# Optimization experiments

Hardware: AMD Instinct MI355X
Metric: run time of the kernel (lower is better)

The kernel has to match this reference:

```python
import jax, jax.numpy as jnp
import numpy as np

EMBED_DIM = 1024
NUM_HEADS = 16
ROTARY_THETA = 10000.0


def _rotate_half(t):
    d = t.shape[-1] // 2
    t1, t2 = t[..., :d], t[..., d:]
    return jnp.concatenate([-t2, t1], axis=-1)


def _rope_cos_sin(seq_len, head_dim, dtype):
    # inv_freq over even indices, standard RoPE
    inv_freq = 1.0 / (ROTARY_THETA ** (jnp.arange(0, head_dim, 2, dtype=jnp.float32) / head_dim))
    freqs = jnp.arange(seq_len, dtype=jnp.float32)[:, None] * inv_freq[None, :]  # (S, D/2)
    emb = jnp.concatenate([freqs, freqs], axis=-1)  # (S, D)
    # broadcast over (b, s, h, d)
    return jnp.cos(emb).astype(dtype)[None, :, None, :], jnp.sin(emb).astype(dtype)[None, :, None, :]


def setup_inputs() -> dict:
    key = jax.random.key(0)
    ks = jax.random.split(key, 4)
    B, S, E = 2, 2048, EMBED_DIM
    scale = 1.0 / np.sqrt(E)
    return {
        "x": jax.random.normal(ks[0], (B, S, E), dtype=jnp.float32),
        "attention_mask": jnp.zeros((B, 1, 1, S), dtype=jnp.float32),
        "Wq": jax.random.normal(ks[1], (E, E), dtype=jnp.float32) * scale,
        "bq": jnp.zeros((E,), dtype=jnp.float32),
        "Wk": jax.random.normal(ks[2], (E, E), dtype=jnp.float32) * scale,
        "bk": jnp.zeros((E,), dtype=jnp.float32),
        "Wv": jax.random.normal(ks[3], (E, E), dtype=jnp.float32) * scale,
        "bv": jnp.zeros((E,), dtype=jnp.float32),
    }


def reference(x, attention_mask, Wq, bq, Wk, bk, Wv, bv):
    B, S, E = x.shape
    H = NUM_HEADS
    D = E // H

    q = (x @ Wq + bq).reshape(B, S, H, D)
    k = (x @ Wk + bk).reshape(B, S, H, D)
    v = (x @ Wv + bv).reshape(B, S, H, D)

    cos, sin = _rope_cos_sin(S, D, q.dtype)
    q = q * cos + _rotate_half(q) * sin
    k = k * cos + _rotate_half(k) * sin

    # attention_mask: additive padding bias (b,1,1,k) broadcast over heads & queries
    scores = jnp.einsum("bqhd,bkhd->bhqk", q, k) / jnp.sqrt(jnp.asarray(D, dtype=q.dtype))
    scores = scores + attention_mask  # broadcasts to (b,h,q,k)
    attn = jax.nn.softmax(scores, axis=-1)
    out = jnp.einsum("bhqk,bkhd->bqhd", attn, v)
    return out.reshape(B, S, E)
```

## Files before the change

### kernel.cpp

```cpp
#include <hip/hip_runtime.h>

typedef __attribute__((ext_vector_type(8)))  short bf16x8;
typedef __attribute__((ext_vector_type(4)))  float f32x4;
typedef __attribute__((ext_vector_type(16))) float f32x16;
typedef __attribute__((ext_vector_type(4)))  unsigned u32x4;
typedef __attribute__((ext_vector_type(4)))  _Float16 f16x4;

#define B_  2
#define S_  2048
#define H_  16
#define D_  64
#define E_  1024
#define M_  (B_*S_)
#define L2E 1.44269504f

__device__ __forceinline__ unsigned short f2bf(float f){
  unsigned x = __builtin_bit_cast(unsigned, f);
  x += 0x7fffu + ((x >> 16) & 1u);
  return (unsigned short)(x >> 16);
}
__device__ __forceinline__ unsigned pk_bf16(float lo, float hi){
  unsigned short a = __builtin_bit_cast(unsigned short, (__bf16)lo);
  unsigned short b = __builtin_bit_cast(unsigned short, (__bf16)hi);
  return (unsigned)a | ((unsigned)b << 16);
}

#define GLD16(gp, lp) __builtin_amdgcn_global_load_lds( \
    (const __attribute__((address_space(1))) unsigned*)(gp), \
    (__attribute__((address_space(3))) unsigned*)(lp), 16, 0, 0)

__global__ __launch_bounds__(256) void k_tables(const float* __restrict__ mask,
                                                float* ct, float* st, float* maskC){
  int i = blockIdx.x*256 + threadIdx.x;
  int s = i >> 5, f = i & 31;
  float invf = powf(10000.0f, -(float)f / 32.0f);
  float ph = (float)s * invf;
  ct[i] = cosf(ph);
  st[i] = sinf(ph);
  if(i < B_*S_) maskC[i] = fmaf(mask[i], L2E, -17.0f);
}

__global__ __launch_bounds__(256) void k_cvt(const float* __restrict__ in, short* __restrict__ out){
  int i = (blockIdx.x*256 + threadIdx.x)*4;
  float4 v = *(const float4*)(in + i);
  typedef __attribute__((ext_vector_type(4))) short s16x4;
  s16x4 o = { (short)f2bf(v.x), (short)f2bf(v.y), (short)f2bf(v.z), (short)f2bf(v.w) };
  *(s16x4*)(out + i) = o;
}

__global__ __launch_bounds__(256) void k_wt(const float* __restrict__ Wq, const float* __restrict__ Wk,
                                            const float* __restrict__ Wv, short* __restrict__ wt){
  const float* W = blockIdx.z==0 ? Wq : (blockIdx.z==1 ? Wk : Wv);
  short* out = wt + (size_t)blockIdx.z*E_*E_;
  __shared__ short tile[64][72];
  int nb = blockIdx.x*64, kb = blockIdx.y*64;
  int t = threadIdx.x;
  {
    int r = t>>2, c0 = (t&3)*16;
    const float* src = W + (size_t)(kb+r)*E_ + nb + c0;
    #pragma unroll
    for(int i=0;i<4;i++){
      float4 v = *(const float4*)(src + i*4);
      tile[r][c0+i*4+0] = (short)f2bf(v.x);
      tile[r][c0+i*4+1] = (short)f2bf(v.y);
      tile[r][c0+i*4+2] = (short)f2bf(v.z);
      tile[r][c0+i*4+3] = (short)f2bf(v.w);
    }
  }
  __syncthreads();
  {
    int n = t>>2, k0 = (t&3)*16;
    short* dst = out + (size_t)(nb+n)*E_ + kb + k0;
    bf16x8 o0, o1;
    #pragma unroll
    for(int i=0;i<8;i++){ o0[i] = tile[k0+i][n]; o1[i] = tile[k0+8+i][n]; }
    *(bf16x8*)dst = o0;
    *(bf16x8*)(dst+8) = o1;
  }
}

__global__ __launch_bounds__(256) void k_gemm(const short* __restrict__ A, const short* __restrict__ WT,
                                              const float* __restrict__ biasq, const float* __restrict__ biask,
                                              const float* __restrict__ biasv,
                                              short* __restrict__ oq, short* __restrict__ ok, short* __restrict__ ov,
                                              const float* __restrict__ cost, const float* __restrict__ sint){
  const int z = blockIdx.z;
  const short* Bw = WT + (size_t)z*E_*E_;
  const float* bias = z==0 ? biasq : (z==1 ? biask : biasv);
  short* out = z==0 ? oq : (z==1 ? ok : ov);
  __shared__ short As[128*32];
  __shared__ short Bs[128*32];
  const int t = threadIdx.x, lane = t & 63, wid = t >> 6;
  const int mb = blockIdx.x*128, nb = blockIdx.y*128;
  const int wm = (wid>>1)*64, wn = (wid&1)*64;
  f32x4 acc[4][4] = {};
  for(int kt=0; kt<E_/32; kt++){
    __syncthreads();
    {
      int f0 = t, f1 = t + 256;
      GLD16(A  + (size_t)(mb + (f0>>2))*E_ + kt*32 + (f0&3)*8, &As[f0*8]);
      GLD16(A  + (size_t)(mb + (f1>>2))*E_ + kt*32 + (f1&3)*8, &As[f1*8]);
      GLD16(Bw + (size_t)(nb + (f0>>2))*E_ + kt*32 + (f0&3)*8, &Bs[f0*8]);
      GLD16(Bw + (size_t)(nb + (f1>>2))*E_ + kt*32 + (f1&3)*8, &Bs[f1*8]);
    }
    __syncthreads();
    bf16x8 af[4], bfv[4];
    #pragma unroll
    for(int mf=0; mf<4; mf++)
      af[mf] = *(const bf16x8*)&As[(wm + mf*16 + (lane&15))*32 + (lane>>4)*8];
    #pragma unroll
    for(int nf=0; nf<4; nf++)
      bfv[nf] = *(const bf16x8*)&Bs[(wn + nf*16 + (lane&15))*32 + (lane>>4)*8];
    #pragma unroll
    for(int mf=0; mf<4; mf++)
      #pragma unroll
      for(int nf=0; nf<4; nf++)
        acc[mf][nf] = __builtin_amdgcn_mfma_f32_16x16x32_bf16(af[mf], bfv[nf], acc[mf][nf], 0, 0, 0);
  }
  const int col16 = lane & 15, rg = lane >> 4;
  float bvs[4];
  #pragma unroll
  for(int nf=0; nf<4; nf++) bvs[nf] = bias[nb + wn + nf*16 + col16];
  if(z == 2){
    #pragma unroll
    for(int mf=0; mf<4; mf++)
      #pragma unroll
      for(int nf=0; nf<4; nf++)
        #pragma unroll
        for(int r=0; r<4; r++){
          int row = mb + wm + mf*16 + rg*4 + r;
          out[(size_t)row*E_ + nb + wn + nf*16 + col16] = (short)f2bf(acc[mf][nf][r] + bvs[nf]);
        }
  } else {
    const float qs = (z==0) ? (0.125f*L2E) : 1.0f;
    #pragma unroll
    for(int mf=0; mf<4; mf++)
      #pragma unroll
      for(int r=0; r<4; r++){
        int row = mb + wm + mf*16 + rg*4 + r;
        int srow = row & (S_-1);
        const float* cb = cost + (size_t)srow*32;
        const float* sb = sint + (size_t)srow*32;
        #pragma unroll
        for(int nf=0; nf<2; nf++){
          int d = nf*16 + col16;
          float c = cb[d], sn = sb[d];
          float x0 = acc[mf][nf][r]   + bvs[nf];
          float x1 = acc[mf][nf+2][r] + bvs[nf+2];
          out[(size_t)row*E_ + nb + wn + nf*16 + col16]     = (short)f2bf((x0*c - x1*sn)*qs);
          out[(size_t)row*E_ + nb + wn + (nf+2)*16 + col16] = (short)f2bf((x1*c + x0*sn)*qs);
        }
      }
  }
}

__global__ __launch_bounds__(256) void k_vt(const short* __restrict__ v, short* __restrict__ vt){
  __shared__ short tl[64][72];
  const int b = blockIdx.z, h = blockIdx.y, s0 = blockIdx.x*64;
  const int t = threadIdx.x;
  {
    int r = t>>2, c0 = (t&3)*16;
    const short* src = v + ((size_t)(b*S_ + s0 + r)*H_ + h)*D_ + c0;
    *(bf16x8*)&tl[r][c0]   = *(const bf16x8*)src;
    *(bf16x8*)&tl[r][c0+8] = *(const bf16x8*)(src+8);
  }
  __syncthreads();
  {
    int d = t>>2, t0 = (t&3)*16;
    short* dst = vt + ((size_t)(b*H_ + h)*D_ + d)*S_ + s0 + t0;
    bf16x8 o0, o1;
    #pragma unroll
    for(int i=0;i<8;i++){ o0[i] = tl[t0+i][d]; o1[i] = tl[t0+8+i][d]; }
    *(bf16x8*)dst = o0;
    *(bf16x8*)(dst+8) = o1;
  }
}

__global__ __launch_bounds__(256,4) void k_attn(
    const short* __restrict__ qg, const short* __restrict__ kg,
    const short* __restrict__ vtg, const float* __restrict__ maskC,
    float* __restrict__ o0g, _Float16* __restrict__ o1g, float* __restrict__ lpart){
  __shared__ short Ks[2][64*72];
  __shared__ short Vs[2][64*72];
  const int b = blockIdx.z, h = blockIdx.y;
  const int qb = blockIdx.x >> 1, sp = blockIdx.x & 1;
  const int tid = threadIdx.x, wid = tid>>6, lane = tid&63;
  const int l31 = lane & 31, hl = lane >> 5;
  const int qw = qb*128 + wid*32;
  const int rr = tid>>3, ch = tid&7;
  const int kb0 = sp*16;
  const int NT = 16;

  bf16x8 qf[4];
  {
    const short* qp = qg + ((size_t)(b*S_ + qw + l31)*H_ + h)*D_;
    #pragma unroll
    for(int dk=0; dk<4; dk++)
      qf[dk] = *(const bf16x8*)(qp + dk*16 + hl*8);
  }
  f32x16 O0 = {}, O1 = {};
  float l_run = 0.f;
  const float* mrow = maskC + (size_t)b*S_;

  bf16x8 ka, kc, va, vc;
#define LOADT(kb) { \
    const short* ks_ = kg + ((size_t)(b*S_ + (kb)*64 + rr)*H_ + h)*D_ + ch*8; \
    ka = *(const bf16x8*)ks_;  kc = *(const bf16x8*)(ks_ + 32*H_*D_); \
    const short* vs_ = vtg + ((size_t)(b*H_ + h)*D_ + rr)*S_ + (kb)*64 + ch*8; \
    va = *(const bf16x8*)vs_;  vc = *(const bf16x8*)(vs_ + 32*S_); }
#define WRITET(pp) { \
    *(bf16x8*)&Ks[pp][rr*72 + ch*8]      = ka; \
    *(bf16x8*)&Ks[pp][(rr+32)*72 + ch*8] = kc; \
    *(bf16x8*)&Vs[pp][rr*72 + ch*8]      = va; \
    *(bf16x8*)&Vs[pp][(rr+32)*72 + ch*8] = vc; }

  LOADT(kb0);
  WRITET(0);
  LOADT(kb0+1);
  __syncthreads();

  int p = 0;
  for(int tt=0; tt<NT; tt++){
    f32x16 s0 = {}, s1 = {};
    #pragma unroll
    for(int dk=0; dk<4; dk++){
      bf16x8 kf0 = *(const bf16x8*)&Ks[p][(l31)*72 + dk*16 + hl*8];
      bf16x8 kf1 = *(const bf16x8*)&Ks[p][(32+l31)*72 + dk*16 + hl*8];
      s0 = __builtin_amdgcn_mfma_f32_32x32x16_bf16(kf0, qf[dk], s0, 0,0,0);
      s1 = __builtin_amdgcn_mfma_f32_32x32x16_bf16(kf1, qf[dk], s1, 0,0,0);
    }
    {
      const float* mt = mrow + (kb0+tt)*64 + hl*4;
      #pragma unroll
      for(int bb=0; bb<4; bb++){
        f32x4 mv0 = *(const f32x4*)(mt + bb*8);
        f32x4 mv1 = *(const f32x4*)(mt + 32 + bb*8);
        #pragma unroll
        for(int a=0; a<4; a++){ s0[bb*4+a] += mv0[a]; s1[bb*4+a] += mv1[a]; }
      }
    }
    #pragma unroll
    for(int i=0;i<16;i++) s0[i] = __builtin_amdgcn_exp2f(s0[i]);
    #pragma unroll
    for(int i=0;i<16;i++) s1[i] = __builtin_amdgcn_exp2f(s1[i]);
    float la=0.f, lb=0.f, lc=0.f, ld=0.f;
    #pragma unroll
    for(int i=0;i<4;i++){
      la += s0[i];   lb += s0[4+i];  lc += s0[8+i];  ld += s0[12+i];
      la += s1[i];   lb += s1[4+i];  lc += s1[8+i];  ld += s1[12+i];
    }
    float ls = (la+lb)+(lc+ld);
    ls += __shfl_xor(ls, 32);
    l_run += ls;

    unsigned w0a[8], w1a[8];
    #pragma unroll
    for(int c=0;c<8;c++){
      int base = (c&3)*4;
      float p0 = (c & 4) ? s1[base+0] : s0[base+0];
      float p1 = (c & 4) ? s1[base+1] : s0[base+1];
      float p2 = (c & 4) ? s1[base+2] : s0[base+2];
      float p3 = (c & 4) ? s1[base+3] : s0[base+3];
      w0a[c] = pk_bf16(p0, p1);
      w1a[c] = pk_bf16(p2, p3);
    }

    if(tt+1 < NT){
      WRITET(p^1);
      if(tt+2 < NT) LOADT(kb0+tt+2);
    }

    #pragma unroll
    for(int ksl=0; ksl<4; ksl++){
      unsigned a0 = w0a[2*ksl], b0 = w0a[2*ksl+1];
      unsigned a1 = w1a[2*ksl], b1 = w1a[2*ksl+1];
      asm("v_permlane32_swap_b32 %0, %1" : "+v"(a0), "+v"(b0));
      asm("v_permlane32_swap_b32 %0, %1" : "+v"(a1), "+v"(b1));
      u32x4 pw = { a0, a1, b0, b1 };
      bf16x8 pf = __builtin_bit_cast(bf16x8, pw);
      bf16x8 vf0 = *(const bf16x8*)&Vs[p][(l31)*72 + ksl*16 + hl*8];
      bf16x8 vf1 = *(const bf16x8*)&Vs[p][(32+l31)*72 + ksl*16 + hl*8];
      O0 = __builtin_amdgcn_mfma_f32_32x32x16_bf16(pf, vf0, O0, 0,0,0);
      O1 = __builtin_amdgcn_mfma_f32_32x32x16_bf16(pf, vf1, O1, 0,0,0);
    }
    __syncthreads();
    p ^= 1;
  }
#undef LOADT
#undef WRITET

  if(sp == 0){
    #pragma unroll
    for(int bb=0; bb<4; bb++)
      #pragma unroll
      for(int a=0; a<4; a++){
        int qrow = qw + a + 8*bb + 4*hl;
        float* op = o0g + ((size_t)(b*S_ + qrow)*H_ + h)*D_;
        op[l31]      = O0[bb*4+a];
        op[32 + l31] = O1[bb*4+a];
      }
  } else {
    #pragma unroll
    for(int bb=0; bb<4; bb++)
      #pragma unroll
      for(int a=0; a<4; a++){
        int qrow = qw + a + 8*bb + 4*hl;
        _Float16* op = o1g + ((size_t)(b*S_ + qrow)*H_ + h)*D_;
        op[l31]      = (_Float16)O0[bb*4+a];
        op[32 + l31] = (_Float16)O1[bb*4+a];
      }
  }
  if(lane < 32)
    lpart[(size_t)sp*(M_*H_) + (size_t)(b*S_ + qw + l31)*H_ + h] = l_run;
}

__global__ __launch_bounds__(256) void k_comb(float* __restrict__ out, const _Float16* __restrict__ o1,
                                              const float* __restrict__ lpart){
  int i = blockIdx.x*256 + threadIdx.x;
  int idx = i*4;
  int lidx = idx >> 6;
  float linv = 1.f / (lpart[lidx] + lpart[M_*H_ + lidx]);
  f32x4 a = *(f32x4*)(out + idx);
  f16x4 bb = *(const f16x4*)(o1 + idx);
  f32x4 r = { (a[0] + (float)bb[0])*linv, (a[1] + (float)bb[1])*linv,
              (a[2] + (float)bb[2])*linv, (a[3] + (float)bb[3])*linv };
  *(f32x4*)(out + idx) = r;
}

extern "C" void kernel_launch(void* const* d_in, const int* in_sizes, int n_in,
                              void* d_out, int out_size, void* d_ws, size_t ws_size,
                              hipStream_t stream){
  (void)in_sizes; (void)n_in; (void)out_size; (void)ws_size;
  const float* x    = (const float*)d_in[0];
  const float* mask = (const float*)d_in[1];
  const float* Wq   = (const float*)d_in[2];
  const float* bq   = (const float*)d_in[3];
  const float* Wk   = (const float*)d_in[4];
  const float* bk   = (const float*)d_in[5];
  const float* Wv   = (const float*)d_in[6];
  const float* bv   = (const float*)d_in[7];
  float* out = (float*)d_out;
  char* ws = (char*)d_ws;
  float* cost  = (float*)(ws);
  float* sint  = (float*)(ws + (256u<<10));
  float* maskC = (float*)(ws + (512u<<10));
  float* lpart = (float*)(ws + (768u<<10));
  short* xb    = (short*)(ws + (2u<<20));
  short* wt    = (short*)(ws + (10u<<20));
  short* qb    = (short*)(ws + (16u<<20));
  short* kb    = (short*)(ws + (24u<<20));
  short* vb    = (short*)(ws + (32u<<20));
  short* vtb   = xb;
  _Float16* o1 = (_Float16*)vb;

  k_tables<<<dim3(256), dim3(256), 0, stream>>>(mask, cost, sint, maskC);
  k_cvt<<<dim3(4096), dim3(256), 0, stream>>>(x, xb);
  k_wt<<<dim3(16,16,3), dim3(256), 0, stream>>>(Wq, Wk, Wv, wt);
  k_gemm<<<dim3(32,8,3), dim3(256), 0, stream>>>(xb, wt, bq, bk, bv, qb, kb, vb, cost, sint);
  k_vt<<<dim3(32,16,2), dim3(256), 0, stream>>>(vb, vtb);
  k_attn<<<dim3(32,16,2), dim3(256), 0, stream>>>(qb, kb, vtb, maskC, out, o1, lpart);
  k_comb<<<dim3(4096), dim3(256), 0, stream>>>(out, o1, lpart);
}
```

Before: 128.0 us.

## Fuse split-KV attention combine in-block, write V transposed from GEMM, merge prologue kernels

The attention kernel now runs three 256-thread groups per block, each covering about a third of the KV tiles. Partial outputs and row sums are reduced through shared memory, which removes the separate combine kernel and the fp16 partial buffer. The V projection epilogue writes directly in transposed layout, removing the k_vt kernel, and the table setup is folded into the x conversion. The mask transform moves into the attention inner loop. In exchange, the per-group loop is single-buffered with two barriers per tile and the block has 768 threads with a larger shared footprint, which may hurt latency hiding and occupancy.

After: 287.8 us. 2.25x slower.

```diff
diff --git a/kernel.cpp b/kernel.cpp
--- a/kernel.cpp
+++ b/kernel.cpp
@@ -1,10 +1,10 @@
 #include <hip/hip_runtime.h>
 
 typedef __attribute__((ext_vector_type(8)))  short bf16x8;
+typedef __attribute__((ext_vector_type(4)))  short s16x4;
 typedef __attribute__((ext_vector_type(4)))  float f32x4;
 typedef __attribute__((ext_vector_type(16))) float f32x16;
 typedef __attribute__((ext_vector_type(4)))  unsigned u32x4;
-typedef __attribute__((ext_vector_type(4)))  _Float16 f16x4;
 
 #define B_  2
 #define S_  2048
@@ -29,23 +29,20 @@
     (const __attribute__((address_space(1))) unsigned*)(gp), \
     (__attribute__((address_space(3))) unsigned*)(lp), 16, 0, 0)
 
-__global__ __launch_bounds__(256) void k_tables(const float* __restrict__ mask,
-                                                float* ct, float* st, float* maskC){
+__global__ __launch_bounds__(256) void k_cvt(const float* __restrict__ in, short* __restrict__ out,
+                                             float* ct, float* st){
   int i = blockIdx.x*256 + threadIdx.x;
-  int s = i >> 5, f = i & 31;
-  float invf = powf(10000.0f, -(float)f / 32.0f);
-  float ph = (float)s * invf;
-  ct[i] = cosf(ph);
-  st[i] = sinf(ph);
-  if(i < B_*S_) maskC[i] = fmaf(mask[i], L2E, -17.0f);
-}
-
-__global__ __launch_bounds__(256) void k_cvt(const float* __restrict__ in, short* __restrict__ out){
-  int i = (blockIdx.x*256 + threadIdx.x)*4;
-  float4 v = *(const float4*)(in + i);
-  typedef __attribute__((ext_vector_type(4))) short s16x4;
+  if(i < S_*32){
+    int s = i >> 5, f = i & 31;
+    float invf = powf(10000.0f, -(float)f / 32.0f);
+    float ph = (float)s * invf;
+    ct[i] = cosf(ph);
+    st[i] = sinf(ph);
+  }
+  int j = i*4;
+  float4 v = *(const float4*)(in + j);
   s16x4 o = { (short)f2bf(v.x), (short)f2bf(v.y), (short)f2bf(v.z), (short)f2bf(v.w) };
-  *(s16x4*)(out + i) = o;
+  *(s16x4*)(out + j) = o;
 }
 
 __global__ __launch_bounds__(256) void k_wt(const float* __restrict__ Wq, const float* __restrict__ Wk,
@@ -82,12 +79,11 @@
 __global__ __launch_bounds__(256) void k_gemm(const short* __restrict__ A, const short* __restrict__ WT,
                                               const float* __restrict__ biasq, const float* __restrict__ biask,
                                               const float* __restrict__ biasv,
-                                              short* __restrict__ oq, short* __restrict__ ok, short* __restrict__ ov,
+                                              short* __restrict__ oq, short* __restrict__ ok, short* __restrict__ ovt,
                                               const float* __restrict__ cost, const float* __restrict__ sint){
   const int z = blockIdx.z;
   const short* Bw = WT + (size_t)z*E_*E_;
   const float* bias = z==0 ? biasq : (z==1 ? biask : biasv);
-  short* out = z==0 ? oq : (z==1 ? ok : ov);
   __shared__ short As[128*32];
   __shared__ short Bs[128*32];
   const int t = threadIdx.x, lane = t & 63, wid = t >> 6;
@@ -123,15 +119,20 @@
   for(int nf=0; nf<4; nf++) bvs[nf] = bias[nb + wn + nf*16 + col16];
   if(z == 2){
     #pragma unroll
-    for(int mf=0; mf<4; mf++)
-      #pragma unroll
-      for(int nf=0; nf<4; nf++)
-        #pragma unroll
-        for(int r=0; r<4; r++){
-          int row = mb + wm + mf*16 + rg*4 + r;
-          out[(size_t)row*E_ + nb + wn + nf*16 + col16] = (short)f2bf(acc[mf][nf][r] + bvs[nf]);
-        }
+    for(int mf=0; mf<4; mf++){
+      int row0 = mb + wm + mf*16 + rg*4;
+      int bb2 = row0 >> 11, ss = row0 & (S_-1);
+      #pragma unroll
+      for(int nf=0; nf<4; nf++){
+        int e = nb + wn + nf*16 + col16;
+        int hh = e >> 6, dd = e & 63;
+        s16x4 w = { (short)f2bf(acc[mf][nf][0]+bvs[nf]), (short)f2bf(acc[mf][nf][1]+bvs[nf]),
+                    (short)f2bf(acc[mf][nf][2]+bvs[nf]), (short)f2bf(acc[mf][nf][3]+bvs[nf]) };
+        *(s16x4*)(ovt + ((size_t)(bb2*H_+hh)*D_+dd)*S_ + ss) = w;
+      }
+    }
   } else {
+    short* out = (z==0) ? oq : ok;
     const float qs = (z==0) ? (0.125f*L2E) : 1.0f;
     #pragma unroll
     for(int mf=0; mf<4; mf++)
@@ -154,42 +155,21 @@
   }
 }
 
-__global__ __launch_bounds__(256) void k_vt(const short* __restrict__ v, short* __restrict__ vt){
-  __shared__ short tl[64][72];
-  const int b = blockIdx.z, h = blockIdx.y, s0 = blockIdx.x*64;
-  const int t = threadIdx.x;
-  {
-    int r = t>>2, c0 = (t&3)*16;
-    const short* src = v + ((size_t)(b*S_ + s0 + r)*H_ + h)*D_ + c0;
-    *(bf16x8*)&tl[r][c0]   = *(const bf16x8*)src;
-    *(bf16x8*)&tl[r][c0+8] = *(const bf16x8*)(src+8);
-  }
-  __syncthreads();
-  {
-    int d = t>>2, t0 = (t&3)*16;
-    short* dst = vt + ((size_t)(b*H_ + h)*D_ + d)*S_ + s0 + t0;
-    bf16x8 o0, o1;
-    #pragma unroll
-    for(int i=0;i<8;i++){ o0[i] = tl[t0+i][d]; o1[i] = tl[t0+8+i][d]; }
-    *(bf16x8*)dst = o0;
-    *(bf16x8*)(dst+8) = o1;
-  }
-}
-
-__global__ __launch_bounds__(256,4) void k_attn(
+__global__ __launch_bounds__(768, 6) void k_attn(
     const short* __restrict__ qg, const short* __restrict__ kg,
-    const short* __restrict__ vtg, const float* __restrict__ maskC,
-    float* __restrict__ o0g, _Float16* __restrict__ o1g, float* __restrict__ lpart){
-  __shared__ short Ks[2][64*72];
-  __shared__ short Vs[2][64*72];
+    const short* __restrict__ vtg, const float* __restrict__ mask,
+    float* __restrict__ outg){
+  __shared__ short smem[3*2*64*72];
   const int b = blockIdx.z, h = blockIdx.y;
-  const int qb = blockIdx.x >> 1, sp = blockIdx.x & 1;
   const int tid = threadIdx.x, wid = tid>>6, lane = tid&63;
+  const int g = wid>>2, w = wid&3;
   const int l31 = lane & 31, hl = lane >> 5;
-  const int qw = qb*128 + wid*32;
-  const int rr = tid>>3, ch = tid&7;
-  const int kb0 = sp*16;
-  const int NT = 16;
+  const int qw = blockIdx.x*128 + w*32;
+  const int tg = tid & 255, rr = tg>>3, ch = tg&7;
+  const int kb0 = g*11;
+  const int NT  = (g==2) ? 10 : 11;
+  short* Ksg = smem + g*9216;
+  short* Vsg = Ksg + 4608;
 
   bf16x8 qf[4];
   {
@@ -200,7 +180,7 @@
   }
   f32x16 O0 = {}, O1 = {};
   float l_run = 0.f;
-  const float* mrow = maskC + (size_t)b*S_;
+  const float* mrow = mask + (size_t)b*S_;
 
   bf16x8 ka, kc, va, vc;
 #define LOADT(kb) { \
@@ -208,123 +188,123 @@
     ka = *(const bf16x8*)ks_;  kc = *(const bf16x8*)(ks_ + 32*H_*D_); \
     const short* vs_ = vtg + ((size_t)(b*H_ + h)*D_ + rr)*S_ + (kb)*64 + ch*8; \
     va = *(const bf16x8*)vs_;  vc = *(const bf16x8*)(vs_ + 32*S_); }
-#define WRITET(pp) { \
-    *(bf16x8*)&Ks[pp][rr*72 + ch*8]      = ka; \
-    *(bf16x8*)&Ks[pp][(rr+32)*72 + ch*8] = kc; \
-    *(bf16x8*)&Vs[pp][rr*72 + ch*8]      = va; \
-    *(bf16x8*)&Vs[pp][(rr+32)*72 + ch*8] = vc; }
+#define WRITET() { \
+    *(bf16x8*)&Ksg[rr*72 + ch*8]      = ka; \
+    *(bf16x8*)&Ksg[(rr+32)*72 + ch*8] = kc; \
+    *(bf16x8*)&Vsg[rr*72 + ch*8]      = va; \
+    *(bf16x8*)&Vsg[(rr+32)*72 + ch*8] = vc; }
 
   LOADT(kb0);
-  WRITET(0);
-  LOADT(kb0+1);
+  WRITET();
   __syncthreads();
 
-  int p = 0;
-  for(int tt=0; tt<NT; tt++){
-    f32x16 s0 = {}, s1 = {};
-    #pragma unroll
-    for(int dk=0; dk<4; dk++){
-      bf16x8 kf0 = *(const bf16x8*)&Ks[p][(l31)*72 + dk*16 + hl*8];
-      bf16x8 kf1 = *(const bf16x8*)&Ks[p][(32+l31)*72 + dk*16 + hl*8];
-      s0 = __builtin_amdgcn_mfma_f32_32x32x16_bf16(kf0, qf[dk], s0, 0,0,0);
-      s1 = __builtin_amdgcn_mfma_f32_32x32x16_bf16(kf1, qf[dk], s1, 0,0,0);
-    }
-    {
-      const float* mt = mrow + (kb0+tt)*64 + hl*4;
-      #pragma unroll
-      for(int bb=0; bb<4; bb++){
-        f32x4 mv0 = *(const f32x4*)(mt + bb*8);
-        f32x4 mv1 = *(const f32x4*)(mt + 32 + bb*8);
+  for(int tt=0; tt<11; tt++){
+    if(tt+1 < NT) LOADT(kb0+tt+1);
+    if(tt < NT){
+      f32x16 s0 = {}, s1 = {};
+      #pragma unroll
+      for(int dk=0; dk<4; dk++){
+        bf16x8 kf0 = *(const bf16x8*)&Ksg[(l31)*72 + dk*16 + hl*8];
+        bf16x8 kf1 = *(const bf16x8*)&Ksg[(32+l31)*72 + dk*16 + hl*8];
+        s0 = __builtin_amdgcn_mfma_f32_32x32x16_bf16(kf0, qf[dk], s0, 0,0,0);
+        s1 = __builtin_amdgcn_mfma_f32_32x32x16_bf16(kf1, qf[dk], s1, 0,0,0);
+      }
+      {
+        const float* mt = mrow + (kb0+tt)*64 + hl*4;
         #pragma unroll
-        for(int a=0; a<4; a++){ s0[bb*4+a] += mv0[a]; s1[bb*4+a] += mv1[a]; }
-      }
-    }
-    #pragma unroll
-    for(int i=0;i<16;i++) s0[i] = __builtin_amdgcn_exp2f(s0[i]);
-    #pragma unroll
-    for(int i=0;i<16;i++) s1[i] = __builtin_amdgcn_exp2f(s1[i]);
-    float la=0.f, lb=0.f, lc=0.f, ld=0.f;
-    #pragma unroll
-    for(int i=0;i<4;i++){
-      la += s0[i];   lb += s0[4+i];  lc += s0[8+i];  ld += s0[12+i];
-      la += s1[i];   lb += s1[4+i];  lc += s1[8+i];  ld += s1[12+i];
-    }
-    float ls = (la+lb)+(lc+ld);
-    ls += __shfl_xor(ls, 32);
-    l_run += ls;
-
-    unsigned w0a[8], w1a[8];
-    #pragma unroll
-    for(int c=0;c<8;c++){
-      int base = (c&3)*4;
-      float p0 = (c & 4) ? s1[base+0] : s0[base+0];
-      float p1 = (c & 4) ? s1[base+1] : s0[base+1];
-      float p2 = (c & 4) ? s1[base+2] : s0[base+2];
-      float p3 = (c & 4) ? s1[base+3] : s0[base+3];
-      w0a[c] = pk_bf16(p0, p1);
-      w1a[c] = pk_bf16(p2, p3);
-    }
-
-    if(tt+1 < NT){
-      WRITET(p^1);
-      if(tt+2 < NT) LOADT(kb0+tt+2);
-    }
-
-    #pragma unroll
-    for(int ksl=0; ksl<4; ksl++){
-      unsigned a0 = w0a[2*ksl], b0 = w0a[2*ksl+1];
-      unsigned a1 = w1a[2*ksl], b1 = w1a[2*ksl+1];
-      asm("v_permlane32_swap_b32 %0, %1" : "+v"(a0), "+v"(b0));
-      asm("v_permlane32_swap_b32 %0, %1" : "+v"(a1), "+v"(b1));
-      u32x4 pw = { a0, a1, b0, b1 };
-      bf16x8 pf = __builtin_bit_cast(bf16x8, pw);
-      bf16x8 vf0 = *(const bf16x8*)&Vs[p][(l31)*72 + ksl*16 + hl*8];
-      bf16x8 vf1 = *(const bf16x8*)&Vs[p][(32+l31)*72 + ksl*16 + hl*8];
-      O0 = __builtin_amdgcn_mfma_f32_32x32x16_bf16(pf, vf0, O0, 0,0,0);
-      O1 = __builtin_amdgcn_mfma_f32_32x32x16_bf16(pf, vf1, O1, 0,0,0);
-    }
-    __syncthreads();
-    p ^= 1;
+        for(int bb=0; bb<4; bb++){
+          f32x4 mv0 = *(const f32x4*)(mt + bb*8);
+          f32x4 mv1 = *(const f32x4*)(mt + 32 + bb*8);
+          #pragma unroll
+          for(int a=0; a<4; a++){
+            s0[bb*4+a] += fmaf(mv0[a], L2E, -17.0f);
+            s1[bb*4+a] += fmaf(mv1[a], L2E, -17.0f);
+          }
+        }
+      }
+      #pragma unroll
+      for(int i=0;i<16;i++) s0[i] = __builtin_amdgcn_exp2f(s0[i]);
+      #pragma unroll
+      for(int i=0;i<16;i++) s1[i] = __builtin_amdgcn_exp2f(s1[i]);
+      float la=0.f, lb=0.f, lc=0.f, ld=0.f;
+      #pragma unroll
+      for(int i=0;i<4;i++){
+        la += s0[i];   lb += s0[4+i];  lc += s0[8+i];  ld += s0[12+i];
+        la += s1[i];   lb += s1[4+i];  lc += s1[8+i];  ld += s1[12+i];
+      }
+      float ls = (la+lb)+(lc+ld);
+      ls += __shfl_xor(ls, 32);
+      l_run += ls;
+
+      unsigned w0a[8], w1a[8];
+      #pragma unroll
+      for(int c=0;c<8;c++){
+        int base = (c&3)*4;
+        float p0 = (c & 4) ? s1[base+0] : s0[base+0];
+        float p1 = (c & 4) ? s1[base+1] : s0[base+1];
+        float p2 = (c & 4) ? s1[base+2] : s0[base+2];
+        float p3 = (c & 4) ? s1[base+3] : s0[base+3];
+        w0a[c] = pk_bf16(p0, p1);
+        w1a[c] = pk_bf16(p2, p3);
+      }
+      #pragma unroll
+      for(int ksl=0; ksl<4; ksl++){
+        unsigned a0 = w0a[2*ksl], b0 = w0a[2*ksl+1];
+        unsigned a1 = w1a[2*ksl], b1 = w1a[2*ksl+1];
+        asm("v_permlane32_swap_b32 %0, %1" : "+v"(a0), "+v"(b0));
+        asm("v_permlane32_swap_b32 %0, %1" : "+v"(a1), "+v"(b1));
+        u32x4 pw = { a0, a1, b0, b1 };
+        bf16x8 pf = __builtin_bit_cast(bf16x8, pw);
+        bf16x8 vf0 = *(const bf16x8*)&Vsg[(l31)*72 + ksl*16 + hl*8];
+        bf16x8 vf1 = *(const bf16x8*)&Vsg[(32+l31)*72 + ksl*16 + hl*8];
+        O0 = __builtin_amdgcn_mfma_f32_32x32x16_bf16(pf, vf0, O0, 0,0,0);
+        O1 = __builtin_amdgcn_mfma_f32_32x32x16_bf16(pf, vf1, O1, 0,0,0);
+      }
+    }
+    __syncthreads();
+    if(tt+1 < NT) WRITET();
+    __syncthreads();
   }
 #undef LOADT
 #undef WRITET
 
-  if(sp == 0){
+  float* ex  = (float*)smem;
+  float* exl = (float*)smem + 4*32*64;
+  #pragma unroll
+  for(int src=1; src<=2; src++){
+    if(g == src){
+      #pragma unroll
+      for(int r=0;r<16;r++){
+        ex[(w*32 + r)*64 + lane]      = O0[r];
+        ex[(w*32 + 16 + r)*64 + lane] = O1[r];
+      }
+      if(lane < 32) exl[w*32 + lane] = l_run;
+    }
+    __syncthreads();
+    if(g == 0){
+      #pragma unroll
+      for(int r=0;r<16;r++){
+        O0[r] += ex[(w*32 + r)*64 + lane];
+        O1[r] += ex[(w*32 + 16 + r)*64 + lane];
+      }
+      if(lane < 32) l_run += exl[w*32 + lane];
+    }
+    __syncthreads();
+  }
+
+  if(g == 0){
+    float linv = 1.f / l_run;
     #pragma unroll
     for(int bb=0; bb<4; bb++)
       #pragma unroll
       for(int a=0; a<4; a++){
+        float li = __shfl(linv, a + 8*bb + 4*hl);
         int qrow = qw + a + 8*bb + 4*hl;
-        float* op = o0g + ((size_t)(b*S_ + qrow)*H_ + h)*D_;
-        op[l31]      = O0[bb*4+a];
-        op[32 + l31] = O1[bb*4+a];
-      }
-  } else {
-    #pragma unroll
-    for(int bb=0; bb<4; bb++)
-      #pragma unroll
-      for(int a=0; a<4; a++){
-        int qrow = qw + a + 8*bb + 4*hl;
-        _Float16* op = o1g + ((size_t)(b*S_ + qrow)*H_ + h)*D_;
-        op[l31]      = (_Float16)O0[bb*4+a];
-        op[32 + l31] = (_Float16)O1[bb*4+a];
-      }
-  }
-  if(lane < 32)
-    lpart[(size_t)sp*(M_*H_) + (size_t)(b*S_ + qw + l31)*H_ + h] = l_run;
-}
-
-__global__ __launch_bounds__(256) void k_comb(float* __restrict__ out, const _Float16* __restrict__ o1,
-                                              const float* __restrict__ lpart){
-  int i = blockIdx.x*256 + threadIdx.x;
-  int idx = i*4;
-  int lidx = idx >> 6;
-  float linv = 1.f / (lpart[lidx] + lpart[M_*H_ + lidx]);
-  f32x4 a = *(f32x4*)(out + idx);
-  f16x4 bb = *(const f16x4*)(o1 + idx);
-  f32x4 r = { (a[0] + (float)bb[0])*linv, (a[1] + (float)bb[1])*linv,
-              (a[2] + (float)bb[2])*linv, (a[3] + (float)bb[3])*linv };
-  *(f32x4*)(out + idx) = r;
+        float* op = outg + ((size_t)(b*S_ + qrow)*H_ + h)*D_;
+        op[l31]      = O0[bb*4+a] * li;
+        op[32 + l31] = O1[bb*4+a] * li;
+      }
+  }
 }
 
 extern "C" void kernel_launch(void* const* d_in, const int* in_sizes, int n_in,
@@ -341,23 +321,16 @@
   const float* bv   = (const float*)d_in[7];
   float* out = (float*)d_out;
   char* ws = (char*)d_ws;
-  float* cost  = (float*)(ws);
-  float* sint  = (float*)(ws + (256u<<10));
-  float* maskC = (float*)(ws + (512u<<10));
-  float* lpart = (float*)(ws + (768u<<10));
-  short* xb    = (short*)(ws + (2u<<20));
-  short* wt    = (short*)(ws + (10u<<20));
-  short* qb    = (short*)(ws + (16u<<20));
-  short* kb    = (short*)(ws + (24u<<20));
-  short* vb    = (short*)(ws + (32u<<20));
-  short* vtb   = xb;
-  _Float16* o1 = (_Float16*)vb;
-
-  k_tables<<<dim3(256), dim3(256), 0, stream>>>(mask, cost, sint, maskC);
-  k_cvt<<<dim3(4096), dim3(256), 0, stream>>>(x, xb);
+  float* cost = (float*)(ws);
+  float* sint = (float*)(ws + (256u<<10));
+  short* xb   = (short*)(ws + (512u<<10));
+  short* wt   = (short*)(ws + (8704u<<10));
+  short* qb   = (short*)(ws + (14848u<<10));
+  short* kb   = (short*)(ws + (23040u<<10));
+  short* vtb  = (short*)(ws + (31232u<<10));
+
+  k_cvt<<<dim3(4096), dim3(256), 0, stream>>>(x, xb, cost, sint);
   k_wt<<<dim3(16,16,3), dim3(256), 0, stream>>>(Wq, Wk, Wv, wt);
-  k_gemm<<<dim3(32,8,3), dim3(256), 0, stream>>>(xb, wt, bq, bk, bv, qb, kb, vb, cost, sint);
-  k_vt<<<dim3(32,16,2), dim3(256), 0, stream>>>(vb, vtb);
-  k_attn<<<dim3(32,16,2), dim3(256), 0, stream>>>(qb, kb, vtb, maskC, out, o1, lpart);
-  k_comb<<<dim3(4096), dim3(256), 0, stream>>>(out, o1, lpart);
-}
+  k_gemm<<<dim3(32,8,3), dim3(256), 0, stream>>>(xb, wt, bq, bk, bv, qb, kb, vtb, cost, sint);
+  k_attn<<<dim3(16,16,2), dim3(768), 0, stream>>>(qb, kb, vtb, mask, out);
+}
```
